# Kernel tuning notes

Measured on AMD Instinct MI355X. Metric: run time of the kernel, lower is better.

## Reference

```python
import jax, jax.numpy as jnp
import numpy as np

GAMMA = 1.0

def setup_inputs() -> dict:
    key = jax.random.key(0)
    kx, ky = jax.random.split(key)
    x = jax.random.normal(kx, (8192, 256), dtype=jnp.float32)
    y = jax.random.normal(ky, (8192, 256), dtype=jnp.float32)
    return {"x": x, "y": y}

def reference(x, y):
    # RBF kernel K[i,j] = exp(-gamma * ||x_i - y_j||^2)
    # materializing the O(N*M*D) broadcast difference tensor.
    x2 = jnp.sum(x * x, axis=-1)            # [N]
    y2 = jnp.sum(y * y, axis=-1)            # [M]
    xy = jnp.einsum('nd,md->nm', x, y)      # [N, M] GEMM
    dist2 = x2[:, None] + y2[None, :] - 2.0 * xy
    dist2 = jnp.maximum(dist2, 0.0)         # guard tiny negative round-off
    return jnp.exp(-GAMMA * dist2)
```

## Files before the change

### kernel.cpp

```cpp
#include <hip/hip_runtime.h>


#define M_DIM 8192
#define K_DIM 256
#define BM 64
#define BN 64

typedef long frag8;
typedef __attribute__((ext_vector_type(4))) float float4v;

__global__ __launch_bounds__(256) void prep_kernel(
        const float* __restrict__ x, const float* __restrict__ y,
        unsigned char* __restrict__ xb, unsigned char* __restrict__ yb,
        float* __restrict__ x2, float* __restrict__ y2) {
    int row  = blockIdx.x * 4 + (threadIdx.x >> 6);
    int lane = threadIdx.x & 63;

    const float* src; unsigned char* dst; float* nrm; int r;
    if (row < M_DIM) { src = x; dst = xb; nrm = x2; r = row; }
    else             { src = y; dst = yb; nrm = y2; r = row - M_DIM; }

    const float4* s4 = (const float4*)(src + (size_t)r * K_DIM);
    float4 v = s4[lane];
    float ss = v.x * v.x + v.y * v.y + v.z * v.z + v.w * v.w;

    int packed = __builtin_amdgcn_cvt_pk_fp8_f32(v.x, v.y, 0, false);
    packed     = __builtin_amdgcn_cvt_pk_fp8_f32(v.z, v.w, packed, true);

    int u  = lane >> 2;
    int su = u ^ (r & 15);
    *(unsigned int*)(dst + (size_t)r * 256 + su * 16 + (lane & 3) * 4) =
        (unsigned int)packed;

    #pragma unroll
    for (int o = 32; o > 0; o >>= 1) ss += __shfl_down(ss, o);
    if (lane == 0) nrm[r] = ss;
}

__global__ __launch_bounds__(256, 4) void rbf_gemm(
        const unsigned char* __restrict__ xb, const unsigned char* __restrict__ yb,
        const float* __restrict__ x2, const float* __restrict__ y2,
        float* __restrict__ out) {
    __shared__ __align__(16) unsigned char As[BM * 256];
    __shared__ __align__(16) unsigned char Bs[BN * 256];

    const int tid  = threadIdx.x;
    const int wid  = tid >> 6;
    const int lane = tid & 63;
    const int wm   = wid >> 1;
    const int wn   = wid & 1;

    const int bid = blockIdx.x;
    const int xcd = bid & 7;
    const int lin = bid >> 3;
    const int ty  = (xcd << 4) + (lin >> 7);
    const int tx  = lin & 127;
    const int m0  = ty * BM;
    const int n0  = tx * BN;

    #pragma unroll
    for (int i = 0; i < 4; ++i) {
        const int ch = wid * 4 + i;
        __builtin_amdgcn_global_load_lds(
            (__attribute__((address_space(1))) void*)
                (xb + (size_t)(m0 + ch * 4) * 256 + lane * 16),
            (__attribute__((address_space(3))) void*)&As[ch * 1024],
            16, 0, 0);
    }
    #pragma unroll
    for (int i = 0; i < 4; ++i) {
        const int ch = wid * 4 + i;
        __builtin_amdgcn_global_load_lds(
            (__attribute__((address_space(1))) void*)
                (yb + (size_t)(n0 + ch * 4) * 256 + lane * 16),
            (__attribute__((address_space(3))) void*)&Bs[ch * 1024],
            16, 0, 0);
    }
    __syncthreads();

    const int fr = lane & 15;
    const int g  = lane >> 4;

    float4v acc[2][2] = {};

    #pragma unroll
    for (int ks = 0; ks < 8; ++ks) {
        const int off = (((2 * ks + (g >> 1)) ^ fr) << 4) + (g & 1) * 8;
        frag8 a[2], b[2];
        #pragma unroll
        for (int mt = 0; mt < 2; ++mt)
            a[mt] = *(const frag8*)&As[(wm * 32 + mt * 16 + fr) * 256 + off];
        #pragma unroll
        for (int nt = 0; nt < 2; ++nt)
            b[nt] = *(const frag8*)&Bs[(wn * 32 + nt * 16 + fr) * 256 + off];
        #pragma unroll
        for (int mt = 0; mt < 2; ++mt)
            #pragma unroll
            for (int nt = 0; nt < 2; ++nt)
                acc[mt][nt] = __builtin_amdgcn_mfma_f32_16x16x32_fp8_fp8(
                    a[mt], b[nt], acc[mt][nt], 0, 0, 0);
    }

    const int q = lane >> 4;
    const int c = lane & 15;
    #pragma unroll
    for (int mt = 0; mt < 2; ++mt) {
        const int rowb = m0 + wm * 32 + mt * 16 + q * 4;
        float x2v[4];
        #pragma unroll
        for (int v = 0; v < 4; ++v) x2v[v] = x2[rowb + v];
        #pragma unroll
        for (int nt = 0; nt < 2; ++nt) {
            const int col = n0 + wn * 32 + nt * 16 + c;
            const float y2v = y2[col];
            #pragma unroll
            for (int v = 0; v < 4; ++v) {
                float d = x2v[v] + y2v - 2.0f * acc[mt][nt][v];
                d = fmaxf(d, 0.0f);
                float r = 0.0f;
                if (__ballot(d < 105.0f) != 0ULL)
                    r = (d < 105.0f) ? __expf(-d) : 0.0f;
                out[(size_t)(rowb + v) * M_DIM + col] = r;
            }
        }
    }
}

__global__ void rbf_naive(const float* __restrict__ x, const float* __restrict__ y,
                          float* __restrict__ out) {
    __shared__ float xs[16][17];
    __shared__ float ys[16][17];
    const int tx = threadIdx.x, ty = threadIdx.y;
    const int row = blockIdx.y * 16 + ty;
    const int col = blockIdx.x * 16 + tx;
    float acc = 0.0f;
    for (int k0 = 0; k0 < K_DIM; k0 += 16) {
        xs[ty][tx] = x[(size_t)row * K_DIM + k0 + tx];
        ys[ty][tx] = y[(size_t)(blockIdx.x * 16 + ty) * K_DIM + k0 + tx];
        __syncthreads();
        #pragma unroll
        for (int kk = 0; kk < 16; ++kk) {
            float d = xs[ty][kk] - ys[tx][kk];
            acc += d * d;
        }
        __syncthreads();
    }
    out[(size_t)row * M_DIM + col] = __expf(-acc);
}

extern "C" void kernel_launch(void* const* d_in, const int* in_sizes, int n_in,
                              void* d_out, int out_size, void* d_ws, size_t ws_size,
                              hipStream_t stream) {
    const float* x = (const float*)d_in[0];
    const float* y = (const float*)d_in[1];
    float* out = (float*)d_out;

    const size_t need = (size_t)2 * M_DIM * 256
                      + (size_t)2 * M_DIM * sizeof(float);
    if (ws_size >= need) {
        unsigned char* xb = (unsigned char*)d_ws;
        unsigned char* yb = xb + (size_t)M_DIM * 256;
        float* x2 = (float*)(yb + (size_t)M_DIM * 256);
        float* y2 = x2 + M_DIM;

        prep_kernel<<<dim3((2 * M_DIM) / 4), dim3(256), 0, stream>>>(x, y, xb, yb, x2, y2);
        rbf_gemm<<<dim3((M_DIM / BM) * (M_DIM / BN)), dim3(256), 0, stream>>>(xb, yb, x2, y2, out);
    } else {
        rbf_naive<<<dim3(M_DIM / 16, M_DIM / 16), dim3(16, 16), 0, stream>>>(x, y, out);
    }
}
```

Before: 282.1 us.

## Stage RBF output through LDS for coalesced nontemporal float4 stores with 32x128 tiles

Changes the block tile from 64x64 to 32x128 and has each wave compute a 16x64 strip sharing one A fragment across four MFMAs. After computing exp results, the kernel writes them to an LDS transpose buffer (reusing the operand smem) and then emits row-contiguous float4 nontemporal stores instead of scattered 4-byte stores. Norm loads are hoisted before the barrier so they overlap the async global-to-LDS copies. This targets the output write bandwidth that dominates a 256 MB fp32 result, at the cost of extra barriers and LDS traffic.

```diff
diff --git a/kernel.cpp b/kernel.cpp
--- a/kernel.cpp
+++ b/kernel.cpp
@@ -3,8 +3,9 @@
 
 #define M_DIM 8192
 #define K_DIM 256
-#define BM 64
-#define BN 64
+#define BM 32
+#define BN 128
+#define TRS 144
 
 typedef long frag8;
 typedef __attribute__((ext_vector_type(4))) float float4v;
@@ -41,8 +42,10 @@
         const unsigned char* __restrict__ xb, const unsigned char* __restrict__ yb,
         const float* __restrict__ x2, const float* __restrict__ y2,
         float* __restrict__ out) {
-    __shared__ __align__(16) unsigned char As[BM * 256];
-    __shared__ __align__(16) unsigned char Bs[BN * 256];
+    __shared__ __align__(16) unsigned char smem[(BM + BN) * 256];
+    unsigned char* As = smem;
+    unsigned char* Bs = smem + BM * 256;
+    float* T = (float*)smem;
 
     const int tid  = threadIdx.x;
     const int wid  = tid >> 6;
@@ -53,14 +56,14 @@
     const int bid = blockIdx.x;
     const int xcd = bid & 7;
     const int lin = bid >> 3;
-    const int ty  = (xcd << 4) + (lin >> 7);
-    const int tx  = lin & 127;
+    const int ty  = (xcd << 5) + (lin >> 6);
+    const int tx  = lin & 63;
     const int m0  = ty * BM;
     const int n0  = tx * BN;
 
     #pragma unroll
-    for (int i = 0; i < 4; ++i) {
-        const int ch = wid * 4 + i;
+    for (int i = 0; i < 2; ++i) {
+        const int ch = wid * 2 + i;
         __builtin_amdgcn_global_load_lds(
             (__attribute__((address_space(1))) void*)
                 (xb + (size_t)(m0 + ch * 4) * 256 + lane * 16),
@@ -68,61 +71,70 @@
             16, 0, 0);
     }
     #pragma unroll
-    for (int i = 0; i < 4; ++i) {
-        const int ch = wid * 4 + i;
+    for (int i = 0; i < 8; ++i) {
+        const int ch = wid * 8 + i;
         __builtin_amdgcn_global_load_lds(
             (__attribute__((address_space(1))) void*)
                 (yb + (size_t)(n0 + ch * 4) * 256 + lane * 16),
             (__attribute__((address_space(3))) void*)&Bs[ch * 1024],
             16, 0, 0);
     }
+
+    const int q = lane >> 4;
+    const int c = lane & 15;
+    float x2v[4];
+    #pragma unroll
+    for (int v = 0; v < 4; ++v)
+        x2v[v] = x2[m0 + wm * 16 + q * 4 + v];
+    float y2v[4];
+    #pragma unroll
+    for (int nt = 0; nt < 4; ++nt)
+        y2v[nt] = y2[n0 + wn * 64 + nt * 16 + c];
+
     __syncthreads();
 
     const int fr = lane & 15;
     const int g  = lane >> 4;
 
-    float4v acc[2][2] = {};
+    float4v acc[4] = {};
 
     #pragma unroll
     for (int ks = 0; ks < 8; ++ks) {
         const int off = (((2 * ks + (g >> 1)) ^ fr) << 4) + (g & 1) * 8;
-        frag8 a[2], b[2];
+        const frag8 a = *(const frag8*)&As[(wm * 16 + fr) * 256 + off];
         #pragma unroll
-        for (int mt = 0; mt < 2; ++mt)
-            a[mt] = *(const frag8*)&As[(wm * 32 + mt * 16 + fr) * 256 + off];
-        #pragma unroll
-        for (int nt = 0; nt < 2; ++nt)
-            b[nt] = *(const frag8*)&Bs[(wn * 32 + nt * 16 + fr) * 256 + off];
-        #pragma unroll
-        for (int mt = 0; mt < 2; ++mt)
-            #pragma unroll
-            for (int nt = 0; nt < 2; ++nt)
-                acc[mt][nt] = __builtin_amdgcn_mfma_f32_16x16x32_fp8_fp8(
-                    a[mt], b[nt], acc[mt][nt], 0, 0, 0);
+        for (int nt = 0; nt < 4; ++nt) {
+            const frag8 b = *(const frag8*)&Bs[(wn * 64 + nt * 16 + fr) * 256 + off];
+            acc[nt] = __builtin_amdgcn_mfma_f32_16x16x32_fp8_fp8(
+                a, b, acc[nt], 0, 0, 0);
+        }
     }
 
-    const int q = lane >> 4;
-    const int c = lane & 15;
+    __syncthreads();
+
     #pragma unroll
-    for (int mt = 0; mt < 2; ++mt) {
-        const int rowb = m0 + wm * 32 + mt * 16 + q * 4;
-        float x2v[4];
+    for (int nt = 0; nt < 4; ++nt) {
         #pragma unroll
-        for (int v = 0; v < 4; ++v) x2v[v] = x2[rowb + v];
-        #pragma unroll
-        for (int nt = 0; nt < 2; ++nt) {
-            const int col = n0 + wn * 32 + nt * 16 + c;
-            const float y2v = y2[col];
-            #pragma unroll
-            for (int v = 0; v < 4; ++v) {
-                float d = x2v[v] + y2v - 2.0f * acc[mt][nt][v];
-                d = fmaxf(d, 0.0f);
-                float r = 0.0f;
-                if (__ballot(d < 105.0f) != 0ULL)
-                    r = (d < 105.0f) ? __expf(-d) : 0.0f;
-                out[(size_t)(rowb + v) * M_DIM + col] = r;
-            }
+        for (int v = 0; v < 4; ++v) {
+            float d = x2v[v] + y2v[nt] - 2.0f * acc[nt][v];
+            d = fmaxf(d, 0.0f);
+            float r = 0.0f;
+            if (__ballot(d < 105.0f) != 0ULL)
+                r = (d < 105.0f) ? __expf(-d) : 0.0f;
+            T[(wm * 16 + q * 4 + v) * TRS + wn * 64 + nt * 16 + c] = r;
         }
+    }
+
+    __syncthreads();
+
+    const int rl = lane >> 5;
+    const int cl = lane & 31;
+    #pragma unroll
+    for (int i = 0; i < 4; ++i) {
+        const int r2 = wid * 8 + i * 2 + rl;
+        float4v val = *(const float4v*)&T[r2 * TRS + cl * 4];
+        __builtin_nontemporal_store(val,
+            (float4v*)&out[(size_t)(m0 + r2) * M_DIM + n0 + cl * 4]);
     }
 }
 
```

Result: slower. 289.2 us (+2.5%).
